# Kernel tuning notes

Measured on AMD Instinct MI355X. Metric: run time of the kernel, lower is better.

The kernel has to match this reference:

```python
import jax, jax.numpy as jnp
import numpy as np

N_SRC = 50000
N_DST = 50000
E = 800000
D = 128
OUT = 128


def setup_inputs() -> dict:
    key = jax.random.key(0)
    k1, k2, k3, k4, k5, k6 = jax.random.split(key, 6)
    lim = 1.0 / np.sqrt(D)
    return {
        "x_src": jax.random.normal(k1, (N_SRC, D), dtype=jnp.float32),
        "x_dst": jax.random.normal(k2, (N_DST, D), dtype=jnp.float32),
        "edge_src": jax.random.randint(k3, (E,), 0, N_SRC, dtype=jnp.int64),
        "edge_dst": jax.random.randint(k4, (E,), 0, N_DST, dtype=jnp.int64),
        "num_dst": N_DST,
        # learned params (torch nn.Linear: y = x @ W.T + b), stored here as [in, out]
        "W_neigh": jax.random.uniform(k5, (D, OUT), jnp.float32, -lim, lim),
        "b_neigh": jnp.zeros((OUT,), jnp.float32),
        "W_self": jax.random.uniform(k6, (D, OUT), jnp.float32, -lim, lim),
        "b_self": jnp.zeros((OUT,), jnp.float32),
    }


def reference(x_src, x_dst, edge_src, edge_dst, num_dst, W_neigh, b_neigh, W_self, b_self):
    # gather source features per edge: [E, D]
    neigh_feats = x_src[edge_src]
    # scatter-mean onto destination nodes
    summed = jax.ops.segment_sum(neigh_feats, edge_dst, num_segments=num_dst)  # [num_dst, D]
    count = jax.ops.segment_sum(jnp.ones((edge_dst.shape[0], 1), x_src.dtype), edge_dst,
                                num_segments=num_dst)
    agg = summed / jnp.clip(count, 1.0)
    # dual linear + add
    return agg @ W_neigh + b_neigh + x_dst @ W_self + b_self
```

## Files before the change

kernel.cpp:

```cpp
#include <hip/hip_runtime.h>

#define D 128
#define TM 64
#define CBITS 7
#define CSIZE 128
#define MAXNB 512
#define CAPB 2560

typedef __attribute__((ext_vector_type(8))) short bf16x8;
typedef __attribute__((ext_vector_type(4))) float f32x4;


__device__ __forceinline__ unsigned short f32_to_bf16(float x) {
    unsigned u = __float_as_uint(x);
    u += 0x7FFFu + ((u >> 16) & 1u);
    return (unsigned short)(u >> 16);
}
__device__ __forceinline__ float bf16_to_f32(unsigned short h) {
    return __uint_as_float(((unsigned)h) << 16);
}

__global__ __launch_bounds__(256) void prep_kernel(
    const float* __restrict__ Wn, const float* __restrict__ Ws,
    unsigned short* __restrict__ Wtn, unsigned short* __restrict__ Wts,
    int* __restrict__ gcursor, int NB) {
    const int stride = gridDim.x * 256;
    for (int i = blockIdx.x * 256 + threadIdx.x; i < D * D; i += stride) {
        int n = i >> 7, k = i & (D - 1);
        Wtn[i] = f32_to_bf16(Wn[k * D + n]);
        Wts[i] = f32_to_bf16(Ws[k * D + n]);
    }
    for (int i = blockIdx.x * 256 + threadIdx.x; i < NB; i += stride)
        gcursor[i] = 0;
}

__global__ __launch_bounds__(256) void fused_part_gemm_kernel(
    const int* __restrict__ edge_src, const int* __restrict__ edge_dst,
    int* __restrict__ gcursor, int* __restrict__ packed, int E, int NB,
    const float* __restrict__ x_src, const float* __restrict__ x_dst,
    const unsigned short* __restrict__ Wtn, const unsigned short* __restrict__ Wts,
    const float* __restrict__ bn, const float* __restrict__ bs,
    unsigned short* __restrict__ y16, float* __restrict__ out,
    int M_SRC, int N, int nblk, int blkA, int pstride) {
    __shared__ __align__(16) char smem[TM * 136 * 2];
    const int t = threadIdx.x;
    const int idx = (int)blockIdx.x;

    const bool isPart = (idx % pstride == 0) && (idx / pstride < nblk);

    if (isPart) {
        const int pid = idx / pstride;
        int* lh    = (int*)smem;
        int* lbase = lh + MAXNB;
        for (int i = t; i < NB; i += 256) lh[i] = 0;
        __syncthreads();
        const int base = pid * 2048;
        int es[8], ed[8];
        #pragma unroll
        for (int i = 0; i < 8; ++i) {
            int e = base + t + i * 256;
            if (e < E) { es[i] = edge_src[e]; ed[i] = edge_dst[e]; }
            else ed[i] = -1;
        }
        #pragma unroll
        for (int i = 0; i < 8; ++i)
            if (ed[i] >= 0) atomicAdd(&lh[ed[i] >> CBITS], 1);
        __syncthreads();
        for (int i = t; i < NB; i += 256) {
            int v = lh[i];
            lbase[i] = v ? atomicAdd(&gcursor[i], v) : 0;
        }
        __syncthreads();
        for (int i = t; i < NB; i += 256) lh[i] = 0;
        __syncthreads();
        #pragma unroll
        for (int i = 0; i < 8; ++i) {
            if (ed[i] >= 0) {
                int bk = ed[i] >> CBITS;
                int pos = lbase[bk] + atomicAdd(&lh[bk], 1);
                if (pos < CAPB)
                    packed[(size_t)bk * CAPB + pos] =
                        (es[i] << CBITS) | (ed[i] & (CSIZE - 1));
            }
        }
        return;
    }

    typedef unsigned short ushort136[136];
    ushort136* LA = (ushort136*)smem;

    const int npb  = min((idx + pstride - 1) / pstride, nblk);
    const int gb   = idx - npb;
    const bool isA  = gb < blkA;
    const int  row0 = (isA ? gb : gb - blkA) * TM;
    const int  M    = isA ? M_SRC : N;
    const float* Ap = isA ? x_src : x_dst;
    const unsigned short* Wp = isA ? Wtn : Wts;

    {
        const float4* Av = (const float4*)Ap;
        #pragma unroll
        for (int i = 0; i < 8; ++i) {
            int vi = t + i * 256;
            int r = vi >> 5, c4 = vi & 31;
            int sr = min(row0 + r, M - 1);
            float4 v = Av[(size_t)sr * 32 + c4];
            ushort4 p;
            p.x = f32_to_bf16(v.x); p.y = f32_to_bf16(v.y);
            p.z = f32_to_bf16(v.z); p.w = f32_to_bf16(v.w);
            *(ushort4*)&LA[r][c4 * 4] = p;
        }
    }
    __syncthreads();

    const int lane = t & 63;
    const int wv   = t >> 6;
    const int wr   = wv & 1;
    const int wc   = wv >> 1;
    const int lr   = lane & 15;
    const int g    = lane >> 4;

    f32x4 acc[2][4];
    #pragma unroll
    for (int i = 0; i < 2; ++i)
        #pragma unroll
        for (int j = 0; j < 4; ++j) acc[i][j] = (f32x4){0.f, 0.f, 0.f, 0.f};

    #pragma unroll
    for (int kt = 0; kt < 4; ++kt) {
        const int kk = kt * 32 + g * 8;
        bf16x8 b0 = *(const bf16x8*)&Wp[(size_t)(wc * 64 + 0 * 16 + lr) * D + kk];
        bf16x8 b1 = *(const bf16x8*)&Wp[(size_t)(wc * 64 + 1 * 16 + lr) * D + kk];
        bf16x8 b2 = *(const bf16x8*)&Wp[(size_t)(wc * 64 + 2 * 16 + lr) * D + kk];
        bf16x8 b3 = *(const bf16x8*)&Wp[(size_t)(wc * 64 + 3 * 16 + lr) * D + kk];
        bf16x8 a0 = *(const bf16x8*)&LA[wr * 32 + lr][kk];
        bf16x8 a1 = *(const bf16x8*)&LA[wr * 32 + 16 + lr][kk];
        acc[0][0] = __builtin_amdgcn_mfma_f32_16x16x32_bf16(a0, b0, acc[0][0], 0, 0, 0);
        acc[0][1] = __builtin_amdgcn_mfma_f32_16x16x32_bf16(a0, b1, acc[0][1], 0, 0, 0);
        acc[0][2] = __builtin_amdgcn_mfma_f32_16x16x32_bf16(a0, b2, acc[0][2], 0, 0, 0);
        acc[0][3] = __builtin_amdgcn_mfma_f32_16x16x32_bf16(a0, b3, acc[0][3], 0, 0, 0);
        acc[1][0] = __builtin_amdgcn_mfma_f32_16x16x32_bf16(a1, b0, acc[1][0], 0, 0, 0);
        acc[1][1] = __builtin_amdgcn_mfma_f32_16x16x32_bf16(a1, b1, acc[1][1], 0, 0, 0);
        acc[1][2] = __builtin_amdgcn_mfma_f32_16x16x32_bf16(a1, b2, acc[1][2], 0, 0, 0);
        acc[1][3] = __builtin_amdgcn_mfma_f32_16x16x32_bf16(a1, b3, acc[1][3], 0, 0, 0);
    }

    if (isA) {
        #pragma unroll
        for (int i = 0; i < 2; ++i) {
            #pragma unroll
            for (int j = 0; j < 4; ++j) {
                int col = wc * 64 + j * 16 + lr;
                #pragma unroll
                for (int r = 0; r < 4; ++r) {
                    int row = row0 + wr * 32 + i * 16 + g * 4 + r;
                    if (row < M)
                        y16[(size_t)row * D + col] = f32_to_bf16(acc[i][j][r]);
                }
            }
        }
    } else {
        #pragma unroll
        for (int i = 0; i < 2; ++i) {
            #pragma unroll
            for (int j = 0; j < 4; ++j) {
                int col = wc * 64 + j * 16 + lr;
                float bias = bn[col] + bs[col];
                #pragma unroll
                for (int r = 0; r < 4; ++r) {
                    int row = row0 + wr * 32 + i * 16 + g * 4 + r;
                    if (row < M)
                        out[(size_t)row * D + col] = acc[i][j][r] + bias;
                }
            }
        }
    }
}

__global__ __launch_bounds__(256) void fine_kernel(
    const int* __restrict__ packed, const int* __restrict__ gcursor,
    int* __restrict__ off_beg, int* __restrict__ off_end,
    int* __restrict__ eidx, int N) {
    __shared__ int dcount[4][CSIZE];
    __shared__ int wbase[4][CSIZE];
    __shared__ int sbuf[CSIZE];
    const int b  = blockIdx.x;
    const int d0 = b << CBITS;
    const int beg = b * CAPB;
    const int cnt = min(gcursor[b], CAPB);
    const int t = threadIdx.x;
    const int wv = t >> 6;

    if (t < CSIZE) {
        dcount[0][t] = 0; dcount[1][t] = 0;
        dcount[2][t] = 0; dcount[3][t] = 0;
    }
    __syncthreads();
    for (int i = t; i < cnt; i += 256)
        atomicAdd(&dcount[wv][packed[beg + i] & (CSIZE - 1)], 1);
    __syncthreads();
    int tot = 0;
    if (t < CSIZE) {
        tot = dcount[0][t] + dcount[1][t] + dcount[2][t] + dcount[3][t];
        sbuf[t] = tot;
    }
    __syncthreads();
    for (int ofs = 1; ofs < CSIZE; ofs <<= 1) {
        int u = (t < CSIZE && t >= ofs) ? sbuf[t - ofs] : 0;
        __syncthreads();
        if (t < CSIZE) sbuf[t] += u;
        __syncthreads();
    }
    if (t < CSIZE) {
        int excl = sbuf[t] - tot;
        int d = d0 + t;
        if (d < N) {
            off_beg[d] = beg + excl;
            off_end[d] = beg + excl + tot;
        }
        int run = excl;
        #pragma unroll
        for (int w = 0; w < 4; ++w) {
            wbase[w][t] = run;
            run += dcount[w][t];
        }
    }
    __syncthreads();
    for (int i = t; i < cnt; i += 256) {
        int p = packed[beg + i];
        int pos = beg + atomicAdd(&wbase[wv][p & (CSIZE - 1)], 1);
        eidx[pos] = p >> CBITS;
    }
}

__global__ __launch_bounds__(256) void gather_out_kernel(
    const unsigned short* __restrict__ y16,
    const int* __restrict__ off_beg,
    const int* __restrict__ off_end,
    const int* __restrict__ eidx,
    float* __restrict__ out, int N) {
    const int wave = (int)(((long long)blockIdx.x * blockDim.x + threadIdx.x) >> 6);
    const int lane = threadIdx.x & 63;
    if (wave >= N) return;
    const int h = lane >> 4;
    const int c = lane & 15;
    const int beg = off_beg[wave];
    const int end = off_end[wave];

    float acc[8];
    #pragma unroll
    for (int j = 0; j < 8; ++j) acc[j] = 0.f;

    for (int i = beg + h; i < end; i += 4) {
        int s = eidx[i];
        const int4 v = *reinterpret_cast<const int4*>(y16 + (size_t)s * D + c * 8);
        const unsigned short* hs = (const unsigned short*)&v;
        #pragma unroll
        for (int j = 0; j < 8; ++j) acc[j] += bf16_to_f32(hs[j]);
    }

    #pragma unroll
    for (int j = 0; j < 8; ++j) {
        acc[j] += __shfl_down(acc[j], 32);
        acc[j] += __shfl_down(acc[j], 16);
    }

    if (h == 0) {
        const float inv = 1.0f / fmaxf((float)(end - beg), 1.0f);
        float4* o = reinterpret_cast<float4*>(out + (size_t)wave * D) + c * 2;
        float4 c0 = o[0], c1 = o[1];
        c0.x = fmaf(acc[0], inv, c0.x);
        c0.y = fmaf(acc[1], inv, c0.y);
        c0.z = fmaf(acc[2], inv, c0.z);
        c0.w = fmaf(acc[3], inv, c0.w);
        c1.x = fmaf(acc[4], inv, c1.x);
        c1.y = fmaf(acc[5], inv, c1.y);
        c1.z = fmaf(acc[6], inv, c1.z);
        c1.w = fmaf(acc[7], inv, c1.w);
        o[0] = c0;
        o[1] = c1;
    }
}

extern "C" void kernel_launch(void* const* d_in, const int* in_sizes, int n_in,
                              void* d_out, int out_size, void* d_ws, size_t ws_size,
                              hipStream_t stream) {
    const float* x_src    = (const float*)d_in[0];
    const float* x_dst    = (const float*)d_in[1];
    const int*   edge_src = (const int*)d_in[2];
    const int*   edge_dst = (const int*)d_in[3];
    const float* Wn = (const float*)d_in[5];
    const float* bn = (const float*)d_in[6];
    const float* Ws = (const float*)d_in[7];
    const float* bs = (const float*)d_in[8];

    const int E     = in_sizes[2];
    const int N     = in_sizes[1] / D;
    const int M_SRC = in_sizes[0] / D;

    const int NB   = (N + CSIZE - 1) >> CBITS;
    const int nblk = (E + 2047) / 2048;

    unsigned short* y16 = (unsigned short*)d_ws;
    unsigned short* Wtn = y16 + (size_t)M_SRC * D;
    unsigned short* Wts = Wtn + D * D;
    int* packed  = (int*)(Wts + D * D);
    int* eidx    = packed + (size_t)NB * CAPB;
    int* off_beg = eidx + (size_t)NB * CAPB;
    int* off_end = off_beg + N;
    int* gcursor = off_end + N;

    const int T = 256;
    prep_kernel<<<32, T, 0, stream>>>(Wn, Ws, Wtn, Wts, gcursor, NB);

    const int blkA = (M_SRC + TM - 1) / TM;
    const int blkB = (N + TM - 1) / TM;
    const int total = nblk + blkA + blkB;
    const int pstride = total / nblk > 1 ? total / nblk : 1;
    fused_part_gemm_kernel<<<total, T, 0, stream>>>(
        edge_src, edge_dst, gcursor, packed, E, NB,
        x_src, x_dst, Wtn, Wts, bn, bs, y16, (float*)d_out,
        M_SRC, N, nblk, blkA, pstride);

    fine_kernel<<<NB, T, 0, stream>>>(packed, gcursor, off_beg, off_end, eidx, N);

    gather_out_kernel<<<(N + 3) / 4, T, 0, stream>>>(
        y16, off_beg, off_end, eidx, (float*)d_out, N);
}
```

Baseline: 81.71 us.

## Restructure fused GEMM to per-wave 16-row tiles and double edges per partition block

The GEMM part of the fused kernel no longer stages a 64-row bf16 tile in shared memory. Each wave now independently loads 16 rows of fp32 input straight from global memory, converts them to bf16 in registers, and computes all 128 output columns, which removes the shared-memory staging and block barrier. Partition blocks now handle 4096 edges each instead of 2048 and are placed first in the grid rather than interleaved with GEMM blocks, and launch bounds request 4 blocks per CU. The trade-offs are less reuse of weight loads across rows, more registers for 16 edges per thread, and fewer partition blocks doing more global atomics each.

```diff
diff --git a/kernel.cpp b/kernel.cpp
--- a/kernel.cpp
+++ b/kernel.cpp
@@ -1,11 +1,11 @@
 #include <hip/hip_runtime.h>
 
 #define D 128
-#define TM 64
 #define CBITS 7
 #define CSIZE 128
 #define MAXNB 512
 #define CAPB 2560
+#define EPB 4096
 
 typedef __attribute__((ext_vector_type(8))) short bf16x8;
 typedef __attribute__((ext_vector_type(4))) float f32x4;
@@ -34,36 +34,32 @@
         gcursor[i] = 0;
 }
 
-__global__ __launch_bounds__(256) void fused_part_gemm_kernel(
+__global__ __launch_bounds__(256, 4) void fused_part_gemm_kernel(
     const int* __restrict__ edge_src, const int* __restrict__ edge_dst,
     int* __restrict__ gcursor, int* __restrict__ packed, int E, int NB,
     const float* __restrict__ x_src, const float* __restrict__ x_dst,
     const unsigned short* __restrict__ Wtn, const unsigned short* __restrict__ Wts,
     const float* __restrict__ bn, const float* __restrict__ bs,
     unsigned short* __restrict__ y16, float* __restrict__ out,
-    int M_SRC, int N, int nblk, int blkA, int pstride) {
-    __shared__ __align__(16) char smem[TM * 136 * 2];
+    int M_SRC, int N, int nblk, int wA, int wTot) {
+    __shared__ int lh[MAXNB];
+    __shared__ int lbase[MAXNB];
     const int t = threadIdx.x;
     const int idx = (int)blockIdx.x;
 
-    const bool isPart = (idx % pstride == 0) && (idx / pstride < nblk);
-
-    if (isPart) {
-        const int pid = idx / pstride;
-        int* lh    = (int*)smem;
-        int* lbase = lh + MAXNB;
+    if (idx < nblk) {
         for (int i = t; i < NB; i += 256) lh[i] = 0;
         __syncthreads();
-        const int base = pid * 2048;
-        int es[8], ed[8];
-        #pragma unroll
-        for (int i = 0; i < 8; ++i) {
+        const int base = idx * EPB;
+        int es[16], ed[16];
+        #pragma unroll
+        for (int i = 0; i < 16; ++i) {
             int e = base + t + i * 256;
             if (e < E) { es[i] = edge_src[e]; ed[i] = edge_dst[e]; }
             else ed[i] = -1;
         }
         #pragma unroll
-        for (int i = 0; i < 8; ++i)
+        for (int i = 0; i < 16; ++i)
             if (ed[i] >= 0) atomicAdd(&lh[ed[i] >> CBITS], 1);
         __syncthreads();
         for (int i = t; i < NB; i += 256) {
@@ -74,7 +70,7 @@
         for (int i = t; i < NB; i += 256) lh[i] = 0;
         __syncthreads();
         #pragma unroll
-        for (int i = 0; i < 8; ++i) {
+        for (int i = 0; i < 16; ++i) {
             if (ed[i] >= 0) {
                 int bk = ed[i] >> CBITS;
                 int pos = lbase[bk] + atomicAdd(&lh[bk], 1);
@@ -86,92 +82,67 @@
         return;
     }
 
-    typedef unsigned short ushort136[136];
-    ushort136* LA = (ushort136*)smem;
-
-    const int npb  = min((idx + pstride - 1) / pstride, nblk);
-    const int gb   = idx - npb;
-    const bool isA  = gb < blkA;
-    const int  row0 = (isA ? gb : gb - blkA) * TM;
-    const int  M    = isA ? M_SRC : N;
+    const int w = (idx - nblk) * 4 + (t >> 6);
+    if (w >= wTot) return;
+    const int lane = t & 63;
+    const int lr = lane & 15;
+    const int g  = lane >> 4;
+
+    const bool isA = w < wA;
+    const int  m0  = (isA ? w : w - wA) * 16;
+    const int  M   = isA ? M_SRC : N;
     const float* Ap = isA ? x_src : x_dst;
     const unsigned short* Wp = isA ? Wtn : Wts;
-
-    {
-        const float4* Av = (const float4*)Ap;
-        #pragma unroll
-        for (int i = 0; i < 8; ++i) {
-            int vi = t + i * 256;
-            int r = vi >> 5, c4 = vi & 31;
-            int sr = min(row0 + r, M - 1);
-            float4 v = Av[(size_t)sr * 32 + c4];
-            ushort4 p;
-            p.x = f32_to_bf16(v.x); p.y = f32_to_bf16(v.y);
-            p.z = f32_to_bf16(v.z); p.w = f32_to_bf16(v.w);
-            *(ushort4*)&LA[r][c4 * 4] = p;
-        }
-    }
-    __syncthreads();
-
-    const int lane = t & 63;
-    const int wv   = t >> 6;
-    const int wr   = wv & 1;
-    const int wc   = wv >> 1;
-    const int lr   = lane & 15;
-    const int g    = lane >> 4;
-
-    f32x4 acc[2][4];
+    if (m0 >= M) return;
+
+    const int arow = min(m0 + lr, M - 1);
+    const float4* Arow = (const float4*)(Ap + (size_t)arow * D);
+
+    f32x4 acc[8];
     #pragma unroll
-    for (int i = 0; i < 2; ++i)
-        #pragma unroll
-        for (int j = 0; j < 4; ++j) acc[i][j] = (f32x4){0.f, 0.f, 0.f, 0.f};
+    for (int n = 0; n < 8; ++n) acc[n] = (f32x4){0.f, 0.f, 0.f, 0.f};
 
     #pragma unroll
     for (int kt = 0; kt < 4; ++kt) {
         const int kk = kt * 32 + g * 8;
-        bf16x8 b0 = *(const bf16x8*)&Wp[(size_t)(wc * 64 + 0 * 16 + lr) * D + kk];
-        bf16x8 b1 = *(const bf16x8*)&Wp[(size_t)(wc * 64 + 1 * 16 + lr) * D + kk];
-        bf16x8 b2 = *(const bf16x8*)&Wp[(size_t)(wc * 64 + 2 * 16 + lr) * D + kk];
-        bf16x8 b3 = *(const bf16x8*)&Wp[(size_t)(wc * 64 + 3 * 16 + lr) * D + kk];
-        bf16x8 a0 = *(const bf16x8*)&LA[wr * 32 + lr][kk];
-        bf16x8 a1 = *(const bf16x8*)&LA[wr * 32 + 16 + lr][kk];
-        acc[0][0] = __builtin_amdgcn_mfma_f32_16x16x32_bf16(a0, b0, acc[0][0], 0, 0, 0);
-        acc[0][1] = __builtin_amdgcn_mfma_f32_16x16x32_bf16(a0, b1, acc[0][1], 0, 0, 0);
-        acc[0][2] = __builtin_amdgcn_mfma_f32_16x16x32_bf16(a0, b2, acc[0][2], 0, 0, 0);
-        acc[0][3] = __builtin_amdgcn_mfma_f32_16x16x32_bf16(a0, b3, acc[0][3], 0, 0, 0);
-        acc[1][0] = __builtin_amdgcn_mfma_f32_16x16x32_bf16(a1, b0, acc[1][0], 0, 0, 0);
-        acc[1][1] = __builtin_amdgcn_mfma_f32_16x16x32_bf16(a1, b1, acc[1][1], 0, 0, 0);
-        acc[1][2] = __builtin_amdgcn_mfma_f32_16x16x32_bf16(a1, b2, acc[1][2], 0, 0, 0);
-        acc[1][3] = __builtin_amdgcn_mfma_f32_16x16x32_bf16(a1, b3, acc[1][3], 0, 0, 0);
+        float4 p0 = Arow[kt * 8 + g * 2];
+        float4 p1 = Arow[kt * 8 + g * 2 + 1];
+        bf16x8 a;
+        a[0] = (short)f32_to_bf16(p0.x);
+        a[1] = (short)f32_to_bf16(p0.y);
+        a[2] = (short)f32_to_bf16(p0.z);
+        a[3] = (short)f32_to_bf16(p0.w);
+        a[4] = (short)f32_to_bf16(p1.x);
+        a[5] = (short)f32_to_bf16(p1.y);
+        a[6] = (short)f32_to_bf16(p1.z);
+        a[7] = (short)f32_to_bf16(p1.w);
+        #pragma unroll
+        for (int n = 0; n < 8; ++n) {
+            bf16x8 b = *(const bf16x8*)&Wp[(size_t)(n * 16 + lr) * D + kk];
+            acc[n] = __builtin_amdgcn_mfma_f32_16x16x32_bf16(a, b, acc[n], 0, 0, 0);
+        }
     }
 
     if (isA) {
         #pragma unroll
-        for (int i = 0; i < 2; ++i) {
+        for (int n = 0; n < 8; ++n) {
             #pragma unroll
-            for (int j = 0; j < 4; ++j) {
-                int col = wc * 64 + j * 16 + lr;
-                #pragma unroll
-                for (int r = 0; r < 4; ++r) {
-                    int row = row0 + wr * 32 + i * 16 + g * 4 + r;
-                    if (row < M)
-                        y16[(size_t)row * D + col] = f32_to_bf16(acc[i][j][r]);
-                }
+            for (int r = 0; r < 4; ++r) {
+                int row = m0 + g * 4 + r;
+                if (row < M)
+                    y16[(size_t)row * D + n * 16 + lr] = f32_to_bf16(acc[n][r]);
             }
         }
     } else {
         #pragma unroll
-        for (int i = 0; i < 2; ++i) {
+        for (int n = 0; n < 8; ++n) {
+            int col = n * 16 + lr;
+            float bias = bn[col] + bs[col];
             #pragma unroll
-            for (int j = 0; j < 4; ++j) {
-                int col = wc * 64 + j * 16 + lr;
-                float bias = bn[col] + bs[col];
-                #pragma unroll
-                for (int r = 0; r < 4; ++r) {
-                    int row = row0 + wr * 32 + i * 16 + g * 4 + r;
-                    if (row < M)
-                        out[(size_t)row * D + col] = acc[i][j][r] + bias;
-                }
+            for (int r = 0; r < 4; ++r) {
+                int row = m0 + g * 4 + r;
+                if (row < M)
+                    out[(size_t)row * D + col] = acc[n][r] + bias;
             }
         }
     }
@@ -299,7 +270,7 @@
     const int M_SRC = in_sizes[0] / D;
 
     const int NB   = (N + CSIZE - 1) >> CBITS;
-    const int nblk = (E + 2047) / 2048;
+    const int nblk = (E + EPB - 1) / EPB;
 
     unsigned short* y16 = (unsigned short*)d_ws;
     unsigned short* Wtn = y16 + (size_t)M_SRC * D;
@@ -313,14 +284,14 @@
     const int T = 256;
     prep_kernel<<<32, T, 0, stream>>>(Wn, Ws, Wtn, Wts, gcursor, NB);
 
-    const int blkA = (M_SRC + TM - 1) / TM;
-    const int blkB = (N + TM - 1) / TM;
-    const int total = nblk + blkA + blkB;
-    const int pstride = total / nblk > 1 ? total / nblk : 1;
-    fused_part_gemm_kernel<<<total, T, 0, stream>>>(
+    const int wA   = (M_SRC + 15) / 16;
+    const int wB   = (N + 15) / 16;
+    const int wTot = wA + wB;
+    const int gblk = (wTot + 3) / 4;
+    fused_part_gemm_kernel<<<nblk + gblk, T, 0, stream>>>(
         edge_src, edge_dst, gcursor, packed, E, NB,
         x_src, x_dst, Wtn, Wts, bn, bs, y16, (float*)d_out,
-        M_SRC, N, nblk, blkA, pstride);
+        M_SRC, N, nblk, wA, wTot);
 
     fine_kernel<<<NB, T, 0, stream>>>(packed, gcursor, off_beg, off_end, eidx, N);
 
```

New measurement: 98.94 us. +21.1%, slower.
